# Kernel optimization log

Hardware: AMD Instinct MI355X
Metric: run time of the kernel (lower is better)

## Reference

```python
import jax, jax.numpy as jnp
import numpy as np

EPS = 1e-5
BLEND = 0.5  # with prior_batchsize=0, x_iclm == x_bn so CNM == BatchNorm1d (training mode)


def batchnorm(x, gamma, beta):
    # torch BatchNorm1d training mode: batch mean, biased variance
    mean = x.mean(axis=0)
    var = x.var(axis=0)  # ddof=0 (biased), matching torch normalization
    xn = (x - mean) * jax.lax.rsqrt(var + EPS)
    return xn * gamma + beta


def ensemble_linear(x, W):
    # x: [B, D*F], W: [D, O, F] block-diagonal weights
    B = x.shape[0]
    D, O, F = W.shape
    xb = x.reshape(B, D, F)
    out = jnp.einsum('bdf,dof->bdo', xb, W)
    return out.reshape(B, D * O)


def setup_inputs() -> dict:
    key = jax.random.key(0)
    ks = jax.random.split(key, 3)
    B, F, D, O2 = 16384, 1024, 4, 32
    x = jax.random.normal(ks[0], (B, F), dtype=jnp.float32)
    # torch init: normal_(mean=0, std=0.0001) on linear weights
    W1 = jax.random.normal(ks[1], (D, F, F), dtype=jnp.float32) * 1e-4
    W2 = jax.random.normal(ks[2], (D, O2, F), dtype=jnp.float32) * 1e-4
    g1 = jnp.ones((D * F,), jnp.float32); b1 = jnp.zeros((D * F,), jnp.float32)
    g2 = jnp.ones((D * F,), jnp.float32); b2 = jnp.zeros((D * F,), jnp.float32)
    g3 = jnp.ones((D * O2,), jnp.float32); b3 = jnp.zeros((D * O2,), jnp.float32)
    return {"x": x, "W1": W1, "W2": W2, "g1": g1, "b1": b1,
            "g2": g2, "b2": b2, "g3": g3, "b3": b3}


def reference(x, W1, W2, g1, b1, g2, b2, g3, b3):
    D = W1.shape[0]
    h = jnp.concatenate([x] * D, axis=-1)          # [B, D*F]
    h = batchnorm(h, g1, b1)                        # CNM 1
    h = ensemble_linear(h, W1)                      # EnsembleLinear F->F
    h = jax.nn.sigmoid(batchnorm(h, g2, b2))        # CNM 2 + Sigmoid
    h = ensemble_linear(h, W2)                      # EnsembleLinear F->32
    h = jax.nn.sigmoid(batchnorm(h, g3, b3))        # CNM 3 + Sigmoid
    return h  # [B, D*32]
```

## Files before the change

### kernel.cpp

```cpp
#include <hip/hip_runtime.h>
#include <hip/hip_bf16.h>
#include <stdint.h>

#define B_N 16384
#define F_N 1024
#define D_N 4
#define O_N 32
#define NCOL1 (D_N * F_N)
#define NCOL2 (D_N * O_N)

static constexpr float EPS = 1e-5f;

typedef __bf16 bf16x8 __attribute__((ext_vector_type(8)));
typedef __bf16 bf16x4 __attribute__((ext_vector_type(4)));
typedef float  f32x4  __attribute__((ext_vector_type(4)));

#define GLD16(gp, lp)                                                          \
  __builtin_amdgcn_global_load_lds(                                            \
      (__attribute__((address_space(1))) void*)(uintptr_t)(gp),                \
      (__attribute__((address_space(3))) void*)(lp), 16, 0, 0)

__global__ __launch_bounds__(256) void k_stats_x_conv(
    const float* __restrict__ x, float* __restrict__ part,
    __bf16* __restrict__ xb) {
  int t = threadIdx.x, blk = blockIdx.x;
  const float4* xr = (const float4*)x;
  float s0 = 0, s1 = 0, s2 = 0, s3 = 0, q0 = 0, q1 = 0, q2 = 0, q3 = 0;
  int r0 = blk * 64;
  for (int r = r0; r < r0 + 64; ++r) {
    float4 v = xr[(size_t)r * (F_N / 4) + t];
    s0 += v.x; q0 += v.x * v.x;
    s1 += v.y; q1 += v.y * v.y;
    s2 += v.z; q2 += v.z * v.z;
    s3 += v.w; q3 += v.w * v.w;
    bf16x4 o;
    o[0] = (__bf16)v.x; o[1] = (__bf16)v.y; o[2] = (__bf16)v.z; o[3] = (__bf16)v.w;
    *(bf16x4*)(xb + (size_t)r * F_N + t * 4) = o;
  }
  float* p = part + (size_t)blk * 2048;
  p[t * 4 + 0] = s0; p[t * 4 + 1] = s1; p[t * 4 + 2] = s2; p[t * 4 + 3] = s3;
  p[1024 + t * 4 + 0] = q0; p[1024 + t * 4 + 1] = q1;
  p[1024 + t * 4 + 2] = q2; p[1024 + t * 4 + 3] = q3;
}

__global__ __launch_bounds__(256) void k_stats_x_final(
    const float* __restrict__ part, float* __restrict__ rstdx) {
  int c = blockIdx.x * 256 + threadIdx.x;
  float s = 0, q = 0;
  for (int b = 0; b < 256; ++b) {
    s += part[(size_t)b * 2048 + c];
    q += part[(size_t)b * 2048 + 1024 + c];
  }
  float mean = s * (1.0f / B_N);
  float var = q * (1.0f / B_N) - mean * mean;
  rstdx[c] = rsqrtf(var + EPS);
}

__global__ __launch_bounds__(256) void k_fold_w1(const float* __restrict__ W1,
                                                 const float* __restrict__ g1,
                                                 const float* __restrict__ rstdx,
                                                 __bf16* __restrict__ W1b) {
  size_t base = (size_t)(blockIdx.x * 256 + threadIdx.x) * 4;
  int f = (int)(base & (F_N - 1));
  int d = (int)(base >> 20);
  float4 w = *(const float4*)(W1 + base);
  float4 g = *(const float4*)(g1 + d * F_N + f);
  float4 r = *(const float4*)(rstdx + f);
  bf16x4 o;
  o[0] = (__bf16)(w.x * g.x * r.x); o[1] = (__bf16)(w.y * g.y * r.y);
  o[2] = (__bf16)(w.z * g.z * r.z); o[3] = (__bf16)(w.w * g.w * r.w);
  *(bf16x4*)(W1b + base) = o;
}

__global__ __launch_bounds__(256) void k_fold_w2(const float* __restrict__ W2,
                                                 __bf16* __restrict__ W2b) {
  size_t base = (size_t)(blockIdx.x * 256 + threadIdx.x) * 4;
  float4 w = *(const float4*)(W2 + base);
  bf16x4 o;
  o[0] = (__bf16)w.x; o[1] = (__bf16)w.y; o[2] = (__bf16)w.z; o[3] = (__bf16)w.w;
  *(bf16x4*)(W2b + base) = o;
}

__global__ __launch_bounds__(512, 2) void k_gemm1(
    const __bf16* __restrict__ A, const __bf16* __restrict__ Bw,
    __bf16* __restrict__ C, float* __restrict__ p2s, float* __restrict__ p2q) {
  __shared__ __bf16 ldsA[2][2][256 * 32];
  __shared__ __bf16 ldsB[2][2][256 * 32];
  const int tid = threadIdx.x;
  const int wave = tid >> 6, lane = tid & 63;
  const int wm = wave >> 2, wn = wave & 3;
  int bid = (int)blockIdx.x;
  const int c_ = bid & 7, q_ = bid >> 3;
  const int bm = c_ * 8 + (q_ >> 4), bn = q_ & 15;
  const int m0 = bm * 256, n0 = bn * 256;
  const int fr = lane & 15, kg = lane >> 4;
  const int swz8 = (kg ^ ((fr >> 1) & 3)) * 8;
  const int srow = tid >> 2;
  const int scb = ((tid & 3) ^ ((tid >> 3) & 3)) * 16;
  const char* Ab = (const char*)A + (size_t)(m0 + srow) * (F_N * 2) + scb;
  const char* Bb = (const char*)Bw + (size_t)(n0 + srow) * (F_N * 2) + scb;
  char* ldsAx = (char*)&ldsA[0][0][0];
  char* ldsBx = (char*)&ldsB[0][0][0];
  const int wo = wave * 1024;

#define SA(buf_, kk_, kb_)                                                     \
  do {                                                                         \
    GLD16(Ab + (kb_) + (kk_) * 64,                                             \
          ldsAx + (buf_) * 32768 + (kk_) * 16384 + wo);                        \
    GLD16(Ab + 128 * (F_N * 2) + (kb_) + (kk_) * 64,                           \
          ldsAx + (buf_) * 32768 + (kk_) * 16384 + 8192 + wo);                 \
  } while (0)
#define SBv(buf_, kk_, kb_)                                                    \
  do {                                                                         \
    GLD16(Bb + (kb_) + (kk_) * 64,                                             \
          ldsBx + (buf_) * 32768 + (kk_) * 16384 + wo);                        \
    GLD16(Bb + 128 * (F_N * 2) + (kb_) + (kk_) * 64,                           \
          ldsBx + (buf_) * 32768 + (kk_) * 16384 + 8192 + wo);                 \
  } while (0)
#define LDA4(buf_, kk_, qm_)                                                   \
  { _Pragma("unroll") for (int i_ = 0; i_ < 4; ++i_)                           \
      afr[i_] = *(const bf16x8*)&ldsA[buf_][kk_]                               \
          [(wm * 128 + (qm_) * 64 + i_ * 16 + fr) * 32 + swz8]; }
#define LDB4(buf_, kk_)                                                        \
  { _Pragma("unroll") for (int i_ = 0; i_ < 4; ++i_)                           \
      bfr[i_] = *(const bf16x8*)&ldsB[buf_][kk_]                               \
          [(wn * 64 + i_ * 16 + fr) * 32 + swz8]; }
#define MFMA16(qm_)                                                            \
  { _Pragma("unroll") for (int i_ = 0; i_ < 4; ++i_)                           \
      _Pragma("unroll") for (int j_ = 0; j_ < 4; ++j_)                         \
        acc[(qm_) * 4 + i_][j_] = __builtin_amdgcn_mfma_f32_16x16x32_bf16(     \
            afr[i_], bfr[j_], acc[(qm_) * 4 + i_][j_], 0, 0, 0); }
#define BAR() __builtin_amdgcn_s_barrier()
#define WAITLGKM()                                                             \
  do {                                                                         \
    asm volatile("s_waitcnt lgkmcnt(0)" ::: "memory");                         \
    __builtin_amdgcn_sched_barrier(0);                                         \
  } while (0)
#define WAITVM4() asm volatile("s_waitcnt vmcnt(4)" ::: "memory")
#define PRIO1() __builtin_amdgcn_s_setprio(1)
#define PRIO0() __builtin_amdgcn_s_setprio(0)

  f32x4 acc[8][4] = {};
  bf16x8 afr[4], bfr[4];

  SBv(0, 0, 0); SA(0, 0, 0); SBv(0, 1, 0); SA(0, 1, 0);
  asm volatile("s_waitcnt vmcnt(4)" ::: "memory");
  BAR();

  for (int t = 0; t < 16; t += 2) {
    const int kn1 = (t + 1) * 128;
    const int kn2 = (t + 2 < 16) ? (t + 2) * 128 : 0;
    LDA4(0, 0, 0); LDB4(0, 0); SBv(1, 0, kn1); BAR(); WAITLGKM(); PRIO1(); MFMA16(0); PRIO0(); BAR();
    LDA4(0, 0, 1);             SA (1, 0, kn1); BAR(); WAITLGKM(); PRIO1(); MFMA16(1); PRIO0(); WAITVM4(); BAR();
    LDA4(0, 1, 0); LDB4(0, 1); SBv(1, 1, kn1); BAR(); WAITLGKM(); PRIO1(); MFMA16(0); PRIO0(); BAR();
    LDA4(0, 1, 1);             SA (1, 1, kn1); BAR(); WAITLGKM(); PRIO1(); MFMA16(1); PRIO0(); WAITVM4(); BAR();
    LDA4(1, 0, 0); LDB4(1, 0); SBv(0, 0, kn2); BAR(); WAITLGKM(); PRIO1(); MFMA16(0); PRIO0(); BAR();
    LDA4(1, 0, 1);             SA (0, 0, kn2); BAR(); WAITLGKM(); PRIO1(); MFMA16(1); PRIO0(); WAITVM4(); BAR();
    LDA4(1, 1, 0); LDB4(1, 1); SBv(0, 1, kn2); BAR(); WAITLGKM(); PRIO1(); MFMA16(0); PRIO0(); BAR();
    LDA4(1, 1, 1);             SA (0, 1, kn2); BAR(); WAITLGKM(); PRIO1(); MFMA16(1); PRIO0(); WAITVM4(); BAR();
  }

  const int cr = kg * 4, cc = fr;
#pragma unroll
  for (int mi = 0; mi < 8; ++mi)
#pragma unroll
    for (int ni = 0; ni < 4; ++ni) {
      int row = m0 + wm * 128 + mi * 16 + cr;
      int col = n0 + wn * 64 + ni * 16 + cc;
#pragma unroll
      for (int r = 0; r < 4; ++r)
        C[(size_t)(row + r) * NCOL1 + col] = (__bf16)acc[mi][ni][r];
    }

  float* srs = (float*)&ldsA[1][0][0];
  float* srq = srs + 512;
  __syncthreads();
#pragma unroll
  for (int ni = 0; ni < 4; ++ni) {
    float ss = 0, qq = 0;
#pragma unroll
    for (int mi = 0; mi < 8; ++mi) {
      f32x4 v = acc[mi][ni];
#pragma unroll
      for (int r = 0; r < 4; ++r) { ss += v[r]; qq += v[r] * v[r]; }
    }
    ss += __shfl_xor(ss, 16); ss += __shfl_xor(ss, 32);
    qq += __shfl_xor(qq, 16); qq += __shfl_xor(qq, 32);
    if (lane < 16) {
      srs[wave * 64 + ni * 16 + lane] = ss;
      srq[wave * 64 + ni * 16 + lane] = qq;
    }
  }
  __syncthreads();
  if (tid < 256) {
    int j = tid, wnn = j >> 6, jj = j & 63;
    float S = srs[wnn * 64 + jj] + srs[(4 + wnn) * 64 + jj];
    float Q = srq[wnn * 64 + jj] + srq[(4 + wnn) * 64 + jj];
    p2s[(size_t)bm * NCOL1 + n0 + j] = S;
    p2q[(size_t)bm * NCOL1 + n0 + j] = Q;
  }
#undef SA
#undef SBv
#undef LDA4
#undef LDB4
#undef MFMA16
#undef BAR
#undef WAITLGKM
#undef WAITVM4
#undef PRIO1
#undef PRIO0
}

__global__ __launch_bounds__(256) void k_stats2_final(
    const float* __restrict__ p2s, const float* __restrict__ p2q,
    const float* __restrict__ g2, const float* __restrict__ b2,
    float* __restrict__ a2, float* __restrict__ c2) {
  int c = blockIdx.x * 256 + threadIdx.x;
  float s = 0, q = 0;
  for (int b = 0; b < 64; ++b) {
    s += p2s[(size_t)b * NCOL1 + c];
    q += p2q[(size_t)b * NCOL1 + c];
  }
  float mean = s * (1.0f / B_N);
  float var = q * (1.0f / B_N) - mean * mean;
  float rstd = rsqrtf(var + EPS);
  float aa = rstd * g2[c];
  a2[c] = aa;
  c2[c] = b2[c] - mean * aa;
}

__global__ __launch_bounds__(256) void k_gemm2(
    const __bf16* __restrict__ G1, const __bf16* __restrict__ W2b,
    const float* __restrict__ a2, const float* __restrict__ c2,
    float* __restrict__ out2) {
  const int tid = threadIdx.x;
  const int wave = tid >> 6, lane = tid & 63;
  const int m0 = blockIdx.x * 64;
  const int d = blockIdx.y;
  const int fr = lane & 15, fk = (lane >> 4) * 8;
  const __bf16* Arow = G1 + (size_t)(m0 + wave * 16 + fr) * NCOL1 + d * F_N;
  const __bf16* Wd = W2b + (size_t)d * O_N * F_N;
  const float* ap = a2 + d * F_N;
  const float* cp = c2 + d * F_N;
  f32x4 acc[2] = {};
  for (int k0 = 0; k0 < F_N; k0 += 32) {
    bf16x8 av = *(const bf16x8*)(Arow + k0 + fk);
    f32x4 aa0 = *(const f32x4*)(ap + k0 + fk);
    f32x4 aa1 = *(const f32x4*)(ap + k0 + fk + 4);
    f32x4 cc0 = *(const f32x4*)(cp + k0 + fk);
    f32x4 cc1 = *(const f32x4*)(cp + k0 + fk + 4);
    bf16x8 af;
#pragma unroll
    for (int j = 0; j < 4; ++j) {
      float v = (float)av[j] * aa0[j] + cc0[j];
      af[j] = (__bf16)(1.0f / (1.0f + __expf(-v)));
    }
#pragma unroll
    for (int j = 0; j < 4; ++j) {
      float v = (float)av[4 + j] * aa1[j] + cc1[j];
      af[4 + j] = (__bf16)(1.0f / (1.0f + __expf(-v)));
    }
    bf16x8 b0 = *(const bf16x8*)(Wd + (size_t)fr * F_N + k0 + fk);
    bf16x8 b1 = *(const bf16x8*)(Wd + (size_t)(16 + fr) * F_N + k0 + fk);
    acc[0] = __builtin_amdgcn_mfma_f32_16x16x32_bf16(af, b0, acc[0], 0, 0, 0);
    acc[1] = __builtin_amdgcn_mfma_f32_16x16x32_bf16(af, b1, acc[1], 0, 0, 0);
  }
  const int cr = (lane >> 4) * 4, cc = lane & 15;
#pragma unroll
  for (int n = 0; n < 2; ++n)
#pragma unroll
    for (int r = 0; r < 4; ++r)
      out2[(size_t)(m0 + wave * 16 + cr + r) * NCOL2 + d * O_N + n * 16 + cc] =
          acc[n][r];
}

__global__ __launch_bounds__(128) void k_stats3_partial(
    const float* __restrict__ out2, float* __restrict__ part) {
  int t = threadIdx.x, blk = blockIdx.x;
  float s = 0, q = 0;
  int r0 = blk * 128;
  for (int r = r0; r < r0 + 128; ++r) {
    float v = out2[(size_t)r * NCOL2 + t];
    s += v;
    q += v * v;
  }
  part[(size_t)blk * 256 + t] = s;
  part[(size_t)blk * 256 + 128 + t] = q;
}

__global__ __launch_bounds__(128) void k_stats3_final(
    const float* __restrict__ part, const float* __restrict__ g3,
    const float* __restrict__ b3, float* __restrict__ a3,
    float* __restrict__ c3) {
  int c = threadIdx.x;
  float s = 0, q = 0;
  for (int b = 0; b < 128; ++b) {
    s += part[(size_t)b * 256 + c];
    q += part[(size_t)b * 256 + 128 + c];
  }
  float mean = s * (1.0f / B_N);
  float var = q * (1.0f / B_N) - mean * mean;
  float rstd = rsqrtf(var + EPS);
  float aa = rstd * g3[c];
  a3[c] = aa;
  c3[c] = b3[c] - mean * aa;
}

__global__ __launch_bounds__(256) void k_final(const float* __restrict__ out2,
                                               const float* __restrict__ a3,
                                               const float* __restrict__ c3,
                                               float* __restrict__ out) {
  size_t base = (size_t)(blockIdx.x * 256 + threadIdx.x) * 4;
  int c = (int)(base & (NCOL2 - 1));
  f32x4 v = *(const f32x4*)(out2 + base);
  f32x4 a = *(const f32x4*)(a3 + c);
  f32x4 cc = *(const f32x4*)(c3 + c);
  f32x4 o;
#pragma unroll
  for (int j = 0; j < 4; ++j)
    o[j] = 1.0f / (1.0f + __expf(-(v[j] * a[j] + cc[j])));
  *(f32x4*)(out + base) = o;
}

extern "C" void kernel_launch(void* const* d_in, const int* in_sizes, int n_in,
                              void* d_out, int out_size, void* d_ws,
                              size_t ws_size, hipStream_t stream) {
  (void)in_sizes; (void)n_in; (void)out_size; (void)ws_size;
  const float* x = (const float*)d_in[0];
  const float* W1 = (const float*)d_in[1];
  const float* W2 = (const float*)d_in[2];
  const float* g1 = (const float*)d_in[3];
  const float* g2 = (const float*)d_in[5];
  const float* b2 = (const float*)d_in[6];
  const float* g3 = (const float*)d_in[7];
  const float* b3 = (const float*)d_in[8];
  float* out = (float*)d_out;

  char* ws = (char*)d_ws;
  size_t off = 0;
  auto alloc = [&](size_t bytes) -> void* {
    void* p = ws + off;
    off = (off + bytes + 255) & ~(size_t)255;
    return p;
  };
  float* rstdx = (float*)alloc((size_t)F_N * 4);
  float* a2 = (float*)alloc((size_t)NCOL1 * 4);
  float* c2 = (float*)alloc((size_t)NCOL1 * 4);
  float* a3 = (float*)alloc((size_t)NCOL2 * 4);
  float* c3 = (float*)alloc((size_t)NCOL2 * 4);
  float* part1 = (float*)alloc((size_t)256 * 2048 * 4);
  float* p2s = (float*)alloc((size_t)64 * NCOL1 * 4);
  float* p2q = (float*)alloc((size_t)64 * NCOL1 * 4);
  float* part3 = (float*)alloc((size_t)128 * 256 * 4);
  __bf16* W1b = (__bf16*)alloc((size_t)D_N * F_N * F_N * 2);
  __bf16* W2b = (__bf16*)alloc((size_t)D_N * O_N * F_N * 2);
  __bf16* xb = (__bf16*)alloc((size_t)B_N * F_N * 2);
  __bf16* G1 = (__bf16*)alloc((size_t)B_N * NCOL1 * 2);
  float* out2 = (float*)alloc((size_t)B_N * NCOL2 * 4);

  k_stats_x_conv<<<256, 256, 0, stream>>>(x, part1, xb);
  k_stats_x_final<<<4, 256, 0, stream>>>(part1, rstdx);
  k_fold_w1<<<4096, 256, 0, stream>>>(W1, g1, rstdx, W1b);
  k_fold_w2<<<128, 256, 0, stream>>>(W2, W2b);
  k_gemm1<<<1024, 512, 0, stream>>>(xb, W1b, G1, p2s, p2q);
  k_stats2_final<<<16, 256, 0, stream>>>(p2s, p2q, g2, b2, a2, c2);
  k_gemm2<<<dim3(256, 4), 256, 0, stream>>>(G1, W2b, a2, c2, out2);
  k_stats3_partial<<<128, 128, 0, stream>>>(out2, part3);
  k_stats3_final<<<1, 128, 0, stream>>>(part3, g3, b3, a3, c3);
  k_final<<<2048, 256, 0, stream>>>(out2, a3, c3, out);
}
```

Baseline: 299.5 us.

## Double-buffer MFMA fragment registers to overlap LDS reads with MFMA compute

Splits the A and B register fragments into even and odd sets so that LDS reads for the next sub-step are issued while MFMAs run on the current one. The explicit lgkmcnt(0) waits and about half the barriers are removed from the main GEMM loop, and the first fragments are preloaded before the loop. The aim is to hide LDS latency and cut barrier stalls. The cost is doubled fragment registers and reliance on compiler-inserted waits, which may lower occupancy or reorder the schedule in unwanted ways.

New measurement: 267.3 us. 10.8% less time.

```diff
diff --git a/kernel.cpp b/kernel.cpp
--- a/kernel.cpp
+++ b/kernel.cpp
@@ -117,47 +117,52 @@
     GLD16(Bb + 128 * (F_N * 2) + (kb_) + (kk_) * 64,                           \
           ldsBx + (buf_) * 32768 + (kk_) * 16384 + 8192 + wo);                 \
   } while (0)
-#define LDA4(buf_, kk_, qm_)                                                   \
+#define LDA4(dst_, buf_, kk_, qm_)                                             \
   { _Pragma("unroll") for (int i_ = 0; i_ < 4; ++i_)                           \
-      afr[i_] = *(const bf16x8*)&ldsA[buf_][kk_]                               \
+      dst_[i_] = *(const bf16x8*)&ldsA[buf_][kk_]                              \
           [(wm * 128 + (qm_) * 64 + i_ * 16 + fr) * 32 + swz8]; }
-#define LDB4(buf_, kk_)                                                        \
+#define LDB4(dst_, buf_, kk_)                                                  \
   { _Pragma("unroll") for (int i_ = 0; i_ < 4; ++i_)                           \
-      bfr[i_] = *(const bf16x8*)&ldsB[buf_][kk_]                               \
+      dst_[i_] = *(const bf16x8*)&ldsB[buf_][kk_]                              \
           [(wn * 64 + i_ * 16 + fr) * 32 + swz8]; }
-#define MFMA16(qm_)                                                            \
+#define MFMA16(a_, b_, qm_)                                                    \
   { _Pragma("unroll") for (int i_ = 0; i_ < 4; ++i_)                           \
       _Pragma("unroll") for (int j_ = 0; j_ < 4; ++j_)                         \
         acc[(qm_) * 4 + i_][j_] = __builtin_amdgcn_mfma_f32_16x16x32_bf16(     \
-            afr[i_], bfr[j_], acc[(qm_) * 4 + i_][j_], 0, 0, 0); }
+            a_[i_], b_[j_], acc[(qm_) * 4 + i_][j_], 0, 0, 0); }
 #define BAR() __builtin_amdgcn_s_barrier()
-#define WAITLGKM()                                                             \
-  do {                                                                         \
-    asm volatile("s_waitcnt lgkmcnt(0)" ::: "memory");                         \
-    __builtin_amdgcn_sched_barrier(0);                                         \
-  } while (0)
+#define SB0() __builtin_amdgcn_sched_barrier(0)
 #define WAITVM4() asm volatile("s_waitcnt vmcnt(4)" ::: "memory")
 #define PRIO1() __builtin_amdgcn_s_setprio(1)
 #define PRIO0() __builtin_amdgcn_s_setprio(0)
 
   f32x4 acc[8][4] = {};
-  bf16x8 afr[4], bfr[4];
+  bf16x8 afrE[4], afrO[4], bfrE[4], bfrO[4];
 
   SBv(0, 0, 0); SA(0, 0, 0); SBv(0, 1, 0); SA(0, 1, 0);
   asm volatile("s_waitcnt vmcnt(4)" ::: "memory");
-  BAR();
+  BAR(); SB0();
+  LDA4(afrE, 0, 0, 0); LDB4(bfrE, 0, 0);
+
+#define TILE(b_, nb_, kn_)                                                     \
+  SBv(nb_, 0, kn_); BAR(); SB0();                                              \
+  LDA4(afrO, b_, 0, 1);                                                        \
+  PRIO1(); MFMA16(afrE, bfrE, 0); PRIO0();                                     \
+  SA(nb_, 0, kn_); WAITVM4(); BAR(); SB0();                                    \
+  LDA4(afrE, b_, 1, 0); LDB4(bfrO, b_, 1);                                     \
+  PRIO1(); MFMA16(afrO, bfrE, 1); PRIO0();                                     \
+  SBv(nb_, 1, kn_); BAR(); SB0();                                              \
+  LDA4(afrO, b_, 1, 1);                                                        \
+  PRIO1(); MFMA16(afrE, bfrO, 0); PRIO0();                                     \
+  SA(nb_, 1, kn_); WAITVM4(); BAR(); SB0();                                    \
+  LDA4(afrE, nb_, 0, 0); LDB4(bfrE, nb_, 0);                                   \
+  PRIO1(); MFMA16(afrO, bfrO, 1); PRIO0();
 
   for (int t = 0; t < 16; t += 2) {
     const int kn1 = (t + 1) * 128;
     const int kn2 = (t + 2 < 16) ? (t + 2) * 128 : 0;
-    LDA4(0, 0, 0); LDB4(0, 0); SBv(1, 0, kn1); BAR(); WAITLGKM(); PRIO1(); MFMA16(0); PRIO0(); BAR();
-    LDA4(0, 0, 1);             SA (1, 0, kn1); BAR(); WAITLGKM(); PRIO1(); MFMA16(1); PRIO0(); WAITVM4(); BAR();
-    LDA4(0, 1, 0); LDB4(0, 1); SBv(1, 1, kn1); BAR(); WAITLGKM(); PRIO1(); MFMA16(0); PRIO0(); BAR();
-    LDA4(0, 1, 1);             SA (1, 1, kn1); BAR(); WAITLGKM(); PRIO1(); MFMA16(1); PRIO0(); WAITVM4(); BAR();
-    LDA4(1, 0, 0); LDB4(1, 0); SBv(0, 0, kn2); BAR(); WAITLGKM(); PRIO1(); MFMA16(0); PRIO0(); BAR();
-    LDA4(1, 0, 1);             SA (0, 0, kn2); BAR(); WAITLGKM(); PRIO1(); MFMA16(1); PRIO0(); WAITVM4(); BAR();
-    LDA4(1, 1, 0); LDB4(1, 1); SBv(0, 1, kn2); BAR(); WAITLGKM(); PRIO1(); MFMA16(0); PRIO0(); BAR();
-    LDA4(1, 1, 1);             SA (0, 1, kn2); BAR(); WAITLGKM(); PRIO1(); MFMA16(1); PRIO0(); WAITVM4(); BAR();
+    TILE(0, 1, kn1)
+    TILE(1, 0, kn2)
   }
 
   const int cr = kg * 4, cc = fr;
@@ -204,8 +209,9 @@
 #undef LDA4
 #undef LDB4
 #undef MFMA16
+#undef TILE
 #undef BAR
-#undef WAITLGKM
+#undef SB0
 #undef WAITVM4
 #undef PRIO1
 #undef PRIO0
```
